# Kernel tuning notes

Hardware: AMD Instinct MI355X
Metric: run time of the kernel (lower is better)

The kernel has to match this reference:

```python
import jax, jax.numpy as jnp
import numpy as np

N, K, D, L = 4096, 64, 1024, 16384  # tokens, top-k, d_in, num_latents


def setup_inputs() -> dict:
    key = jax.random.key(0)
    ks = jax.random.split(key, 9)
    x = jax.random.normal(ks[0], (N, D), jnp.float32)
    y = jax.random.normal(ks[1], (N, D), jnp.float32)
    latent_acts = jax.random.uniform(ks[2], (N, K), jnp.float32)  # post-topk acts (nonneg)
    latent_indices = jax.random.randint(ks[3], (N, K), 0, L)
    W_dec = jax.random.normal(ks[4], (L, D), jnp.float32) / np.sqrt(D).astype(np.float32)
    b_dec = jax.random.normal(ks[5], (D,), jnp.float32) * 0.01
    post_enc = jax.random.normal(ks[6], (L,), jnp.float32) * 0.01
    post_enc_scale = 1.0 + 0.1 * jax.random.normal(ks[7], (L,), jnp.float32)
    W_skip = jax.random.normal(ks[8], (D, D), jnp.float32) / np.sqrt(D).astype(np.float32)
    return {
        "x": x, "y": y,
        "latent_acts": latent_acts, "latent_indices": latent_indices,
        "W_dec": W_dec, "b_dec": b_dec,
        "post_enc": post_enc, "post_enc_scale": post_enc_scale,
        "W_skip": W_skip,
    }


def reference(x, y, latent_acts, latent_indices, W_dec, b_dec, post_enc, post_enc_scale, W_skip):
    # current_latent_acts: per-index bias gather + indexed scaling
    acts = (latent_acts + post_enc[latent_indices]) * post_enc_scale[latent_indices]  # [N,K]
    # decode: gather W_dec rows by top-k indices, weighted combine, add decoder bias
    sae_out = jnp.einsum('nk,nkd->nd', acts, W_dec[latent_indices]) + b_dec  # [N,D]
    # skip connection: x @ W_skip.mT
    sae_out = sae_out + x @ W_skip.T
    # FVU loss
    e = y - sae_out
    total_variance = jnp.sum((y - jnp.mean(y, axis=0)) ** 2)
    fvu = jnp.sum(e ** 2) / total_variance
    return sae_out, fvu
```

## Files before the change

kernel.cpp:

```cpp
#include <hip/hip_runtime.h>
#include <hip/hip_bf16.h>
#include <cstdint>

#define N_TOK 4096
#define KTOP  64
#define DIM   1024
#define NLAT  16384

typedef __bf16 bf16x8 __attribute__((ext_vector_type(8)));
typedef float  floatx4 __attribute__((ext_vector_type(4)));

#define GLOBAL_AS(p) ((const __attribute__((address_space(1))) void*)(p))
#define LDS_AS(p)    ((__attribute__((address_space(3))) void*)(p))

__device__ inline unsigned short f2bf(float f){
  unsigned int u = __float_as_uint(f);
  unsigned int r = (u + 0x7fffu + ((u >> 16) & 1u)) >> 16;
  return (unsigned short)r;
}
__device__ inline float bflo(unsigned int u){ return __uint_as_float(u << 16); }
__device__ inline float bfhi(unsigned int u){ return __uint_as_float(u & 0xffff0000u); }

__global__ __launch_bounds__(256) void cvt_bf16_kernel(
    const float* __restrict__ in, unsigned short* __restrict__ out, int n4){
  int i = blockIdx.x * blockDim.x + threadIdx.x;
  if (i >= n4) return;
  float4 v = ((const float4*)in)[i];
  ushort4 o;
  o.x = f2bf(v.x); o.y = f2bf(v.y); o.z = f2bf(v.z); o.w = f2bf(v.w);
  ((ushort4*)out)[i] = o;
}

__global__ __launch_bounds__(256) void skip_gemm(
    const unsigned short* __restrict__ xb,
    const unsigned short* __restrict__ wb,
    const float* __restrict__ b_dec,
    float* __restrict__ out){
  __shared__ unsigned short As[128][32];
  __shared__ unsigned short Bs[128][32];
  const int row0 = blockIdx.x * 128;
  const int col0 = blockIdx.y * 128;
  const int t    = threadIdx.x;
  const int lane = t & 63;
  const int w    = t >> 6;
  const int wr   = (w >> 1) * 64;
  const int wc   = (w & 1) * 64;
  const int lm   = lane & 15;
  const int kq   = lane >> 4;

  const int sr   = t >> 2;
  const int sc   = (t & 3) * 8;

  floatx4 acc[4][4] = {};

  for (int k0 = 0; k0 < DIM; k0 += 32){
    __builtin_amdgcn_global_load_lds(GLOBAL_AS(xb + (size_t)(row0 + sr) * DIM + k0 + sc),
                                     LDS_AS(&As[sr][sc]), 16, 0, 0);
    __builtin_amdgcn_global_load_lds(GLOBAL_AS(xb + (size_t)(row0 + 64 + sr) * DIM + k0 + sc),
                                     LDS_AS(&As[64 + sr][sc]), 16, 0, 0);
    __builtin_amdgcn_global_load_lds(GLOBAL_AS(wb + (size_t)(col0 + sr) * DIM + k0 + sc),
                                     LDS_AS(&Bs[sr][sc]), 16, 0, 0);
    __builtin_amdgcn_global_load_lds(GLOBAL_AS(wb + (size_t)(col0 + 64 + sr) * DIM + k0 + sc),
                                     LDS_AS(&Bs[64 + sr][sc]), 16, 0, 0);
    __syncthreads();
    bf16x8 af[4], bf[4];
    #pragma unroll
    for (int mi = 0; mi < 4; mi++) af[mi] = *(const bf16x8*)(&As[wr + mi * 16 + lm][kq * 8]);
    #pragma unroll
    for (int ni = 0; ni < 4; ni++) bf[ni] = *(const bf16x8*)(&Bs[wc + ni * 16 + lm][kq * 8]);
    #pragma unroll
    for (int mi = 0; mi < 4; mi++)
      #pragma unroll
      for (int ni = 0; ni < 4; ni++)
        acc[mi][ni] = __builtin_amdgcn_mfma_f32_16x16x32_bf16(af[mi], bf[ni], acc[mi][ni], 0, 0, 0);
    __syncthreads();
  }

  const int rq = (lane >> 4) * 4;
  #pragma unroll
  for (int mi = 0; mi < 4; mi++){
    #pragma unroll
    for (int ni = 0; ni < 4; ni++){
      int col = col0 + wc + ni * 16 + lm;
      float bd = b_dec[col];
      #pragma unroll
      for (int r = 0; r < 4; r++){
        int row = row0 + wr + mi * 16 + rq + r;
        out[(size_t)row * DIM + col] = acc[mi][ni][r] + bd;
      }
    }
  }
}

__global__ __launch_bounds__(256) void decode_residual(
    const float* __restrict__ y,
    const float* __restrict__ la,
    const int*   __restrict__ li,
    const unsigned short* __restrict__ Wdb,
    const float* __restrict__ pe,
    const float* __restrict__ pes,
    float* __restrict__ out,
    float* __restrict__ sse){
  const int n0 = blockIdx.x * 2;
  const int t  = threadIdx.x;
  const int half = t >> 7;
  const int lt   = t & 127;
  const int n    = n0 + half;
  __shared__ float s_act[2][KTOP];
  __shared__ int   s_idx[2][KTOP];
  __shared__ float s_red[4];
  if (t < 128){
    int tok = t >> 6, k = t & 63;
    int id = li[(n0 + tok) * KTOP + k];
    s_idx[tok][k] = id;
    s_act[tok][k] = (la[(n0 + tok) * KTOP + k] + pe[id]) * pes[id];
  }
  __syncthreads();
  float* op = out + (size_t)n * DIM + lt * 8;
  float4 o0 = ((const float4*)op)[0], o1 = ((const float4*)op)[1];
  float acc[8] = {o0.x, o0.y, o0.z, o0.w, o1.x, o1.y, o1.z, o1.w};
  #pragma unroll 8
  for (int k = 0; k < KTOP; k++){
    const float a = s_act[half][k];
    const uint4 wv = *(const uint4*)(Wdb + (size_t)s_idx[half][k] * DIM + lt * 8);
    acc[0] += a * bflo(wv.x); acc[1] += a * bfhi(wv.x);
    acc[2] += a * bflo(wv.y); acc[3] += a * bfhi(wv.y);
    acc[4] += a * bflo(wv.z); acc[5] += a * bfhi(wv.z);
    acc[6] += a * bflo(wv.w); acc[7] += a * bfhi(wv.w);
  }
  ((float4*)op)[0] = make_float4(acc[0], acc[1], acc[2], acc[3]);
  ((float4*)op)[1] = make_float4(acc[4], acc[5], acc[6], acc[7]);
  const float* yp = y + (size_t)n * DIM + lt * 8;
  float4 y0 = ((const float4*)yp)[0], y1 = ((const float4*)yp)[1];
  float e0 = y0.x - acc[0], e1 = y0.y - acc[1], e2 = y0.z - acc[2], e3 = y0.w - acc[3];
  float e4 = y1.x - acc[4], e5 = y1.y - acc[5], e6 = y1.z - acc[6], e7 = y1.w - acc[7];
  float s = e0*e0 + e1*e1 + e2*e2 + e3*e3 + e4*e4 + e5*e5 + e6*e6 + e7*e7;
  #pragma unroll
  for (int off = 32; off > 0; off >>= 1) s += __shfl_down(s, off, 64);
  if ((t & 63) == 0) s_red[t >> 6] = s;
  __syncthreads();
  if (t == 0) atomicAdd(sse, s_red[0] + s_red[1] + s_red[2] + s_red[3]);
}

__global__ __launch_bounds__(256) void ystats(
    const float* __restrict__ y, float* __restrict__ colsum, float* __restrict__ sumsq){
  const int t  = threadIdx.x;
  const int r0 = blockIdx.x * 32;
  float4 cs = {0.f, 0.f, 0.f, 0.f};
  float sq = 0.f;
  for (int r = 0; r < 32; r++){
    float4 v = ((const float4*)(y + (size_t)(r0 + r) * DIM))[t];
    cs.x += v.x; cs.y += v.y; cs.z += v.z; cs.w += v.w;
    sq += v.x*v.x + v.y*v.y + v.z*v.z + v.w*v.w;
  }
  atomicAdd(&colsum[t*4+0], cs.x);
  atomicAdd(&colsum[t*4+1], cs.y);
  atomicAdd(&colsum[t*4+2], cs.z);
  atomicAdd(&colsum[t*4+3], cs.w);
  #pragma unroll
  for (int off = 32; off > 0; off >>= 1) sq += __shfl_down(sq, off, 64);
  __shared__ float s_red[4];
  if ((t & 63) == 0) s_red[t >> 6] = sq;
  __syncthreads();
  if (t == 0) atomicAdd(sumsq, s_red[0] + s_red[1] + s_red[2] + s_red[3]);
}

__global__ __launch_bounds__(256) void fvu_kernel(
    const float* __restrict__ ws, float* __restrict__ fvu_out){
  const int t = threadIdx.x;
  float4 c = ((const float4*)(ws + 4))[t];
  float s = c.x*c.x + c.y*c.y + c.z*c.z + c.w*c.w;
  #pragma unroll
  for (int off = 32; off > 0; off >>= 1) s += __shfl_down(s, off, 64);
  __shared__ float s_red[4];
  if ((t & 63) == 0) s_red[t >> 6] = s;
  __syncthreads();
  if (t == 0){
    float ss = s_red[0] + s_red[1] + s_red[2] + s_red[3];
    float tv = ws[1] - ss / (float)N_TOK;
    fvu_out[0] = ws[0] / tv;
  }
}

extern "C" void kernel_launch(void* const* d_in, const int* in_sizes, int n_in,
                              void* d_out, int out_size, void* d_ws, size_t ws_size,
                              hipStream_t stream){
  const float* x   = (const float*)d_in[0];
  const float* y   = (const float*)d_in[1];
  const float* la  = (const float*)d_in[2];
  const int*   li  = (const int*)d_in[3];
  const float* Wd  = (const float*)d_in[4];
  const float* bd  = (const float*)d_in[5];
  const float* pe  = (const float*)d_in[6];
  const float* pes = (const float*)d_in[7];
  const float* Wsk = (const float*)d_in[8];
  float* out = (float*)d_out;

  float* accs = (float*)d_ws;
  unsigned short* xb  = (unsigned short*)((char*)d_ws + 8192);
  unsigned short* wb  = xb + (size_t)N_TOK * DIM;
  unsigned short* wdb = wb + (size_t)DIM * DIM;

  hipMemsetAsync(d_ws, 0, 8192, stream);
  cvt_bf16_kernel<<<N_TOK * DIM / 4 / 256, 256, 0, stream>>>(x,   xb,  N_TOK * DIM / 4);
  cvt_bf16_kernel<<<DIM * DIM / 4 / 256,   256, 0, stream>>>(Wsk, wb,  DIM * DIM / 4);
  cvt_bf16_kernel<<<NLAT * DIM / 4 / 256,  256, 0, stream>>>(Wd,  wdb, NLAT * DIM / 4);
  ystats<<<N_TOK / 32, 256, 0, stream>>>(y, accs + 4, accs + 1);
  skip_gemm<<<dim3(N_TOK / 128, DIM / 128), 256, 0, stream>>>(xb, wb, bd, out);
  decode_residual<<<N_TOK / 2, 256, 0, stream>>>(y, la, li, wdb, pe, pes, out, accs);
  fvu_kernel<<<1, 256, 0, stream>>>(accs, out + (size_t)N_TOK * DIM);
}
```

Measured before the change: 269.7 us.

## Store decoder weights in column-chunked layout and tile decode by chunk

The bf16 copy of W_dec is now written in 8 column chunks of 128 features each, laid out [chunk][latent][128]. The decode kernel gives each block 16 tokens and one chunk, in place of 2 tokens across the full width. The goal is to keep each chunk's gathered rows (4 MB per chunk) resident in L2 across neighbouring blocks and raise cache reuse for the random row gathers. In exchange, each token's index and activation setup is repeated 8 times, and each gather now fetches 256-byte segments instead of 2 KB rows.

```diff
diff --git a/kernel.cpp b/kernel.cpp
--- a/kernel.cpp
+++ b/kernel.cpp
@@ -6,6 +6,7 @@
 #define KTOP  64
 #define DIM   1024
 #define NLAT  16384
+#define NCHUNK 8
 
 typedef __bf16 bf16x8 __attribute__((ext_vector_type(8)));
 typedef float  floatx4 __attribute__((ext_vector_type(4)));
@@ -29,6 +30,18 @@
   ushort4 o;
   o.x = f2bf(v.x); o.y = f2bf(v.y); o.z = f2bf(v.z); o.w = f2bf(v.w);
   ((ushort4*)out)[i] = o;
+}
+
+__global__ __launch_bounds__(256) void cvt_wdec_chunked(
+    const float* __restrict__ Wd, unsigned short* __restrict__ out){
+  const int lat = blockIdx.x;
+  const int t   = threadIdx.x;
+  float4 v = ((const float4*)(Wd + (size_t)lat * DIM))[t];
+  ushort4 o;
+  o.x = f2bf(v.x); o.y = f2bf(v.y); o.z = f2bf(v.z); o.w = f2bf(v.w);
+  const int chunk = t >> 5;
+  const int off   = (t & 31) * 4;
+  *(ushort4*)(out + ((size_t)chunk * NLAT + lat) * 128 + off) = o;
 }
 
 __global__ __launch_bounds__(256) void skip_gemm(
@@ -47,7 +60,6 @@
   const int wc   = (w & 1) * 64;
   const int lm   = lane & 15;
   const int kq   = lane >> 4;
-
   const int sr   = t >> 2;
   const int sc   = (t & 3) * 8;
 
@@ -63,16 +75,16 @@
     __builtin_amdgcn_global_load_lds(GLOBAL_AS(wb + (size_t)(col0 + 64 + sr) * DIM + k0 + sc),
                                      LDS_AS(&Bs[64 + sr][sc]), 16, 0, 0);
     __syncthreads();
-    bf16x8 af[4], bf[4];
+    bf16x8 af[4], bfr[4];
     #pragma unroll
     for (int mi = 0; mi < 4; mi++) af[mi] = *(const bf16x8*)(&As[wr + mi * 16 + lm][kq * 8]);
     #pragma unroll
-    for (int ni = 0; ni < 4; ni++) bf[ni] = *(const bf16x8*)(&Bs[wc + ni * 16 + lm][kq * 8]);
+    for (int ni = 0; ni < 4; ni++) bfr[ni] = *(const bf16x8*)(&Bs[wc + ni * 16 + lm][kq * 8]);
     #pragma unroll
     for (int mi = 0; mi < 4; mi++)
       #pragma unroll
       for (int ni = 0; ni < 4; ni++)
-        acc[mi][ni] = __builtin_amdgcn_mfma_f32_16x16x32_bf16(af[mi], bf[ni], acc[mi][ni], 0, 0, 0);
+        acc[mi][ni] = __builtin_amdgcn_mfma_f32_16x16x32_bf16(af[mi], bfr[ni], acc[mi][ni], 0, 0, 0);
     __syncthreads();
   }
 
@@ -96,33 +108,36 @@
     const float* __restrict__ y,
     const float* __restrict__ la,
     const int*   __restrict__ li,
-    const unsigned short* __restrict__ Wdb,
+    const unsigned short* __restrict__ Wdc,
     const float* __restrict__ pe,
     const float* __restrict__ pes,
     float* __restrict__ out,
     float* __restrict__ sse){
-  const int n0 = blockIdx.x * 2;
+  const int chunk = blockIdx.x & 7;
+  const int tok0  = (blockIdx.x >> 3) * 16;
   const int t  = threadIdx.x;
-  const int half = t >> 7;
-  const int lt   = t & 127;
-  const int n    = n0 + half;
-  __shared__ float s_act[2][KTOP];
-  __shared__ int   s_idx[2][KTOP];
+  const int tl = t >> 4;
+  const int cl = t & 15;
+  __shared__ float s_act[16][KTOP];
+  __shared__ int   s_idx[16][KTOP];
   __shared__ float s_red[4];
-  if (t < 128){
-    int tok = t >> 6, k = t & 63;
-    int id = li[(n0 + tok) * KTOP + k];
-    s_idx[tok][k] = id;
-    s_act[tok][k] = (la[(n0 + tok) * KTOP + k] + pe[id]) * pes[id];
-  }
-  __syncthreads();
-  float* op = out + (size_t)n * DIM + lt * 8;
+  #pragma unroll
+  for (int i = 0; i < 4; i++){
+    int e = t + i * 256;
+    int id = li[(tok0 + (e >> 6)) * KTOP + (e & 63)];
+    s_idx[e >> 6][e & 63] = id;
+    s_act[e >> 6][e & 63] = (la[(tok0 + (e >> 6)) * KTOP + (e & 63)] + pe[id]) * pes[id];
+  }
+  __syncthreads();
+  const int n = tok0 + tl;
+  float* op = out + (size_t)n * DIM + chunk * 128 + cl * 8;
   float4 o0 = ((const float4*)op)[0], o1 = ((const float4*)op)[1];
   float acc[8] = {o0.x, o0.y, o0.z, o0.w, o1.x, o1.y, o1.z, o1.w};
+  const unsigned short* Wc = Wdc + (size_t)chunk * NLAT * 128 + cl * 8;
   #pragma unroll 8
   for (int k = 0; k < KTOP; k++){
-    const float a = s_act[half][k];
-    const uint4 wv = *(const uint4*)(Wdb + (size_t)s_idx[half][k] * DIM + lt * 8);
+    const float a = s_act[tl][k];
+    const uint4 wv = *(const uint4*)(Wc + (size_t)s_idx[tl][k] * 128);
     acc[0] += a * bflo(wv.x); acc[1] += a * bfhi(wv.x);
     acc[2] += a * bflo(wv.y); acc[3] += a * bfhi(wv.y);
     acc[4] += a * bflo(wv.z); acc[5] += a * bfhi(wv.z);
@@ -130,7 +145,7 @@
   }
   ((float4*)op)[0] = make_float4(acc[0], acc[1], acc[2], acc[3]);
   ((float4*)op)[1] = make_float4(acc[4], acc[5], acc[6], acc[7]);
-  const float* yp = y + (size_t)n * DIM + lt * 8;
+  const float* yp = y + (size_t)n * DIM + chunk * 128 + cl * 8;
   float4 y0 = ((const float4*)yp)[0], y1 = ((const float4*)yp)[1];
   float e0 = y0.x - acc[0], e1 = y0.y - acc[1], e2 = y0.z - acc[2], e3 = y0.w - acc[3];
   float e4 = y1.x - acc[4], e5 = y1.y - acc[5], e6 = y1.z - acc[6], e7 = y1.w - acc[7];
@@ -199,14 +214,14 @@
   float* accs = (float*)d_ws;
   unsigned short* xb  = (unsigned short*)((char*)d_ws + 8192);
   unsigned short* wb  = xb + (size_t)N_TOK * DIM;
-  unsigned short* wdb = wb + (size_t)DIM * DIM;
+  unsigned short* wdc = wb + (size_t)DIM * DIM;
 
   hipMemsetAsync(d_ws, 0, 8192, stream);
-  cvt_bf16_kernel<<<N_TOK * DIM / 4 / 256, 256, 0, stream>>>(x,   xb,  N_TOK * DIM / 4);
-  cvt_bf16_kernel<<<DIM * DIM / 4 / 256,   256, 0, stream>>>(Wsk, wb,  DIM * DIM / 4);
-  cvt_bf16_kernel<<<NLAT * DIM / 4 / 256,  256, 0, stream>>>(Wd,  wdb, NLAT * DIM / 4);
+  cvt_bf16_kernel<<<N_TOK * DIM / 4 / 256, 256, 0, stream>>>(x,   xb, N_TOK * DIM / 4);
+  cvt_bf16_kernel<<<DIM * DIM / 4 / 256,   256, 0, stream>>>(Wsk, wb, DIM * DIM / 4);
+  cvt_wdec_chunked<<<NLAT, 256, 0, stream>>>(Wd, wdc);
   ystats<<<N_TOK / 32, 256, 0, stream>>>(y, accs + 4, accs + 1);
   skip_gemm<<<dim3(N_TOK / 128, DIM / 128), 256, 0, stream>>>(xb, wb, bd, out);
-  decode_residual<<<N_TOK / 2, 256, 0, stream>>>(y, la, li, wdb, pe, pes, out, accs);
+  decode_residual<<<(N_TOK / 16) * NCHUNK, 256, 0, stream>>>(y, la, li, wdc, pe, pes, out, accs);
   fvu_kernel<<<1, 256, 0, stream>>>(accs, out + (size_t)N_TOK * DIM);
 }
```

Measured after the change: 242.4 us. 10.1% less time.
